# Kernel optimization log

Measured on AMD Instinct MI355X. Metric: run time of the kernel, lower is better.

## Reference

```python
import jax, jax.numpy as jnp
import numpy as np

NUM_HEADS = 16
HEAD_DIM = 64
D_MODEL = NUM_HEADS * HEAD_DIM


def setup_inputs() -> dict:
    key = jax.random.key(0)
    k1, k2, k3 = jax.random.split(key, 3)
    N, T = 2, 2048
    x = jax.random.normal(k1, (N, T, D_MODEL), dtype=jnp.float32)
    mask = jnp.ones((N, T), dtype=jnp.float32)
    # fused QKV projection params (Dense: H*D*3 outputs)
    W_qkv = jax.random.normal(k2, (D_MODEL, D_MODEL * 3), dtype=jnp.float32) * (D_MODEL ** -0.5)
    b_qkv = jnp.zeros((D_MODEL * 3,), dtype=jnp.float32)
    return {"x": x, "mask": mask, "W_qkv": W_qkv, "b_qkv": b_qkv}


def reference(x, mask, W_qkv, b_qkv):
    N, T, _ = x.shape
    H, D = NUM_HEADS, HEAD_DIM
    qkv = x @ W_qkv + b_qkv                       # [N, T, H*D*3]
    qkv = qkv.reshape(N, T, H, D, 3)
    qkv = jnp.transpose(qkv, (4, 0, 2, 1, 3))     # [3, N, H, T, D]
    q, k, v = qkv[0], qkv[1], qkv[2]
    logits = jnp.einsum('bhqd,bhkd->bhqk', q, k) / (D ** 0.5)  # [N, H, T, T]
    # NOTE: original masks along the QUERY axis (broadcast over keys)
    logits = logits + (1.0 - mask)[:, None, :, None] * -1e9
    w = jax.nn.softmax(logits, axis=-1)
    out = jnp.einsum('bhqk,bhkd->bhqd', w, v)     # [N, H, T, D]
    out = jnp.transpose(out, (0, 2, 1, 3)).reshape(N, T, H * D)
    return out
```

## Files before the change

### kernel.cpp

```cpp
#include <hip/hip_runtime.h>
#include <hip/hip_bf16.h>
#include <stdint.h>

#define NHEADS 16
#define HDIM   64
#define DMODEL 1024
#define SEQ    2048
#define NB     2
#define MTOT   (NB*SEQ)
#define NTOT   (3*DMODEL)
#define KTOT   DMODEL

#define QSCALE 0.18033688011112042f

typedef __attribute__((ext_vector_type(8)))  short          bf16x8;
typedef __attribute__((ext_vector_type(4)))  float          f32x4;
typedef __attribute__((ext_vector_type(8)))  unsigned short u16x8;

__device__ __forceinline__ unsigned short f2bf(float f) {
  unsigned u = __builtin_bit_cast(unsigned, f);
  u += 0x7fffu + ((u >> 16) & 1u);
  return (unsigned short)(u >> 16);
}

__device__ __forceinline__ f32x4 vmax4(f32x4 a, f32x4 b) {
  f32x4 r;
  r[0]=fmaxf(a[0],b[0]); r[1]=fmaxf(a[1],b[1]);
  r[2]=fmaxf(a[2],b[2]); r[3]=fmaxf(a[3],b[3]);
  return r;
}

__device__ __forceinline__ void async_copy16(void* lds, const void* g) {
  __builtin_amdgcn_global_load_lds(
      (const __attribute__((address_space(1))) unsigned int*)g,
      (__attribute__((address_space(3))) unsigned int*)lds, 16, 0, 0);
}

__global__ void convert_x_kernel(const float* __restrict__ x,
                                 unsigned short* __restrict__ xb) {
  int i = blockIdx.x * 256 + threadIdx.x;
  const f32x4* xv = reinterpret_cast<const f32x4*>(x);
  f32x4 a = xv[2*i];
  f32x4 b = xv[2*i + 1];
  u16x8 r;
  r[0]=f2bf(a[0]); r[1]=f2bf(a[1]); r[2]=f2bf(a[2]); r[3]=f2bf(a[3]);
  r[4]=f2bf(b[0]); r[5]=f2bf(b[1]); r[6]=f2bf(b[2]); r[7]=f2bf(b[3]);
  reinterpret_cast<u16x8*>(xb)[i] = r;
}

__global__ void transpose_w_kernel(const float* __restrict__ W,
                                   unsigned short* __restrict__ Wt) {
  __shared__ float tile[64][65];
  int j0 = blockIdx.x * 64;
  int k0 = blockIdx.y * 64;
  int tid = threadIdx.x;
  int lr = tid >> 6;
  int lc = tid & 63;
  #pragma unroll
  for (int i = 0; i < 16; ++i) {
    int r = i*4 + lr;
    tile[r][lc] = W[(size_t)(k0 + r)*NTOT + j0 + lc];
  }
  __syncthreads();
  #pragma unroll
  for (int i = 0; i < 16; ++i) {
    int jr = i*4 + lr;
    int j  = j0 + jr;
    int oc = (j % 3)*DMODEL + (j / 3);
    Wt[(size_t)oc*KTOT + k0 + lc] = f2bf(tile[lc][jr]);
  }
}

#define BM 128
#define BN 128
#define BK2 32
#define NBX (NTOT/BN)
#define NBY (MTOT/BM)
#define EPSTRIDE 136
__launch_bounds__(256)
__global__ void qkv_gemm_kernel(const unsigned short* __restrict__ xb,
                                const unsigned short* __restrict__ wt,
                                const float* __restrict__ bqkv,
                                unsigned short* __restrict__ Qb,
                                unsigned short* __restrict__ Kb,
                                unsigned short* __restrict__ Vt) {
  __shared__ __align__(16) unsigned char gsm[128*EPSTRIDE*2];
  unsigned short* As = (unsigned short*)gsm;
  unsigned short* Bs = (unsigned short*)(gsm + 16384);
  unsigned short* Ep = (unsigned short*)gsm;

  int tid = threadIdx.x;
  int w = tid >> 6, l = tid & 63;
  int m0 = blockIdx.y * BM;
  int n0 = blockIdx.x * BN;
  int ln = l & 15, lg = l >> 4;
  int wm = (w >> 1) * 64;
  int wn = (w & 1) * 64;

  f32x4 acc[4][4];
  const f32x4 zero4 = {0.f, 0.f, 0.f, 0.f};
  #pragma unroll
  for (int i = 0; i < 4; ++i)
    #pragma unroll
    for (int j = 0; j < 4; ++j) acc[i][j] = zero4;

  #define STAGE2(BUF, KT)                                                     \
  do {                                                                        \
    _Pragma("unroll")                                                         \
    for (int i = 0; i < 2; ++i) {                                             \
      int row  = i*64 + w*16 + (l >> 2);                                      \
      int seg  = (l & 3) ^ ((row >> 1) & 3);                                  \
      async_copy16(gsm + (BUF)*8192 + i*4096 + w*1024,                        \
                   &xb[(size_t)(m0 + row)*KTOT + (KT)*BK2 + seg*8]);          \
      async_copy16(gsm + 16384 + (BUF)*8192 + i*4096 + w*1024,                \
                   &wt[(size_t)(n0 + row)*KTOT + (KT)*BK2 + seg*8]);          \
    }                                                                         \
  } while (0)

  STAGE2(0, 0);
  asm volatile("s_waitcnt vmcnt(0)" ::: "memory");
  __syncthreads();

  for (int kt = 0; kt < KTOT/BK2; ++kt) {
    int cur = kt & 1;
    if (kt < KTOT/BK2 - 1) STAGE2(cur ^ 1, kt + 1);

    bf16x8 af[4], bfr[4];
    #pragma unroll
    for (int mi = 0; mi < 4; ++mi) {
      int ra = wm + mi*16 + ln;
      af[mi] = *reinterpret_cast<const bf16x8*>(
          &As[cur*4096 + ra*BK2 + ((lg ^ ((ra >> 1) & 3)) << 3)]);
    }
    #pragma unroll
    for (int ni = 0; ni < 4; ++ni) {
      int rb = wn + ni*16 + ln;
      bfr[ni] = *reinterpret_cast<const bf16x8*>(
          &Bs[cur*4096 + rb*BK2 + ((lg ^ ((rb >> 1) & 3)) << 3)]);
    }
    #pragma unroll
    for (int mi = 0; mi < 4; ++mi)
      #pragma unroll
      for (int ni = 0; ni < 4; ++ni)
        acc[mi][ni] = __builtin_amdgcn_mfma_f32_16x16x32_bf16(af[mi], bfr[ni], acc[mi][ni], 0, 0, 0);

    __syncthreads();
  }
  #undef STAGE2

  int r4 = lg * 4;
  if (n0 >= 2*DMODEL) {
    int hd0 = n0 - 2*DMODEL;
    #pragma unroll
    for (int mi = 0; mi < 4; ++mi) {
      #pragma unroll
      for (int ni = 0; ni < 4; ++ni) {
        int col = wn + ni*16 + ln;
        float bias = bqkv[(hd0 + col)*3 + 2];
        int rb = wm + mi*16 + r4;
        ushort4 pk4;
        pk4.x = f2bf(acc[mi][ni][0] + bias);
        pk4.y = f2bf(acc[mi][ni][1] + bias);
        pk4.z = f2bf(acc[mi][ni][2] + bias);
        pk4.w = f2bf(acc[mi][ni][3] + bias);
        *reinterpret_cast<ushort4*>(&Ep[col*EPSTRIDE + rb]) = pk4;
      }
    }
    __syncthreads();
    int n = m0 >> 11, t0 = m0 & 2047;
    #pragma unroll
    for (int pass = 0; pass < 8; ++pass) {
      int hdl = pass*16 + (tid >> 4);
      int seg = tid & 15;
      bf16x8 v = *reinterpret_cast<const bf16x8*>(&Ep[hdl*EPSTRIDE + seg*8]);
      int hd = hd0 + hdl, h = hd >> 6, d = hd & 63;
      *reinterpret_cast<bf16x8*>(
          &Vt[(((size_t)(n*NHEADS + h)*HDIM + d) << 11) + t0 + seg*8]) = v;
    }
  } else {
    #pragma unroll
    for (int mi = 0; mi < 4; ++mi) {
      #pragma unroll
      for (int ni = 0; ni < 4; ++ni) {
        int nc = n0 + wn + ni*16 + ln;
        int c  = nc >> 10;
        int hd = nc & 1023;
        int h = hd >> 6, d = hd & 63;
        float bias = bqkv[hd*3 + c];
        float qs = (c == 0) ? QSCALE : 1.0f;
        #pragma unroll
        for (int j = 0; j < 4; ++j) {
          int m = m0 + wm + mi*16 + r4 + j;
          int n = m >> 11, t = m & 2047;
          unsigned short val = f2bf((acc[mi][ni][j] + bias) * qs);
          size_t nh = (size_t)(n*NHEADS + h);
          if (c == 0) Qb[((nh*SEQ + t) << 6) + d] = val;
          else        Kb[((nh*SEQ + t) << 6) + d] = val;
        }
      }
    }
  }
}

#define PROW    88
#define POFF    49152
#define PBYTES  2816
#define OREGION 4352
__launch_bounds__(512)
__global__ void attn_kernel(const unsigned short* __restrict__ Qb,
                            const unsigned short* __restrict__ Kb,
                            const unsigned short* __restrict__ Vt,
                            float* __restrict__ out) {
  __shared__ __align__(16) unsigned char smem[POFF + 8*PBYTES];
  int tid = threadIdx.x;
  int w = tid >> 6, l = tid & 63;
  int ln = l & 15, lg = l >> 4;

  unsigned short* Pw  = (unsigned short*)(smem + POFF + w * PBYTES);
  float*          obw = (float*)         (smem + w * OREGION);

  int fid  = blockIdx.x;
  int xcd  = fid & 7, idx = fid >> 3;
  int bh   = xcd * 4 + (idx >> 4);
  int qblk = idx & 15;
  int q0   = qblk * 128 + w * 16;

  const unsigned short* Qh = Qb + (size_t)bh * SEQ * HDIM;
  const unsigned short* Kh = Kb + (size_t)bh * SEQ * HDIM;
  const unsigned short* Vh = Vt + (size_t)bh * HDIM * SEQ;

  int srow = w*8 + (l >> 3);
  int sseg = (l & 7) ^ (srow & 7);

  bf16x8 qf[2];
  #pragma unroll
  for (int dw = 0; dw < 2; ++dw)
    qf[dw] = *reinterpret_cast<const bf16x8*>(&Qh[(size_t)(q0 + ln)*HDIM + dw*32 + lg*8]);

  const f32x4 zero4 = {0.f, 0.f, 0.f, 0.f};
  f32x4 o[4];
  #pragma unroll
  for (int db = 0; db < 4; ++db) o[db] = zero4;
  f32x4 psum4 = zero4;
  float mrow = -INFINITY;
  f32x4 sA[4], sB[4];

  int xorE = (ln & 7) << 3;
  int coff0 = (((     lg*8) ^ xorE)) * 2;
  int coff1 = (((32 + lg*8) ^ xorE)) * 2;
  int rbyte = ln * 128;
  const unsigned char* kv0 = smem + rbyte + coff0;
  const unsigned char* kv1 = smem + rbyte + coff1;

  #define STAGE(BUF, KEY0)                                                    \
  do {                                                                        \
    async_copy16(smem + (BUF)*16384 + w*1024,                                 \
                 &Kh[(size_t)((KEY0) + srow)*HDIM + sseg*8]);                 \
    async_copy16(smem + (BUF)*16384 + 8192 + w*1024,                          \
                 &Vh[(size_t)srow*SEQ + (KEY0) + sseg*8]);                    \
  } while (0)

  #define QKT(CUR, SCUR)                                                      \
  do {                                                                        \
    _Pragma("unroll")                                                         \
    for (int kb = 0; kb < 4; ++kb) {                                          \
      bf16x8 k0 = *reinterpret_cast<const bf16x8*>(kv0 + (CUR)*16384 + kb*2048);\
      bf16x8 k1 = *reinterpret_cast<const bf16x8*>(kv1 + (CUR)*16384 + kb*2048);\
      f32x4 t0 = __builtin_amdgcn_mfma_f32_16x16x32_bf16(k0, qf[0], zero4, 0, 0, 0);\
      SCUR[kb] = __builtin_amdgcn_mfma_f32_16x16x32_bf16(k1, qf[1], t0,    0, 0, 0);\
    }                                                                         \
  } while (0)

  #define SMPV(SPREV, PRV)                                                    \
  do {                                                                        \
    f32x4 m4 = vmax4(vmax4(SPREV[0], SPREV[1]), vmax4(SPREV[2], SPREV[3]));   \
    float localmax = fmaxf(fmaxf(fmaxf(m4[0], m4[1]), m4[2]), m4[3]);         \
    if (!__all(localmax <= mrow + 8.f)) {                                     \
      float pm = localmax;                                                    \
      pm = fmaxf(pm, __shfl_xor(pm, 16));                                     \
      pm = fmaxf(pm, __shfl_xor(pm, 32));                                     \
      float mn  = fmaxf(mrow, pm);                                            \
      float scl = __builtin_amdgcn_exp2f(mrow - mn);                          \
      mrow = mn;                                                              \
      psum4 *= scl;                                                           \
      _Pragma("unroll")                                                       \
      for (int db = 0; db < 4; ++db)                                          \
        _Pragma("unroll")                                                     \
        for (int r = 0; r < 4; ++r) o[db][r] *= scl;                          \
    }                                                                         \
    _Pragma("unroll")                                                         \
    for (int kb = 0; kb < 4; ++kb) {                                          \
      _Pragma("unroll")                                                       \
      for (int r = 0; r < 4; ++r)                                             \
        SPREV[kb][r] = __builtin_amdgcn_exp2f(SPREV[kb][r] - mrow);           \
      psum4 += SPREV[kb];                                                     \
    }                                                                         \
    _Pragma("unroll")                                                         \
    for (int kb = 0; kb < 4; ++kb) {                                          \
      uint2 pk;                                                               \
      asm("v_cvt_pk_bf16_f32 %0, %1, %2" : "=v"(pk.x) : "v"(SPREV[kb][0]), "v"(SPREV[kb][1]));\
      asm("v_cvt_pk_bf16_f32 %0, %1, %2" : "=v"(pk.y) : "v"(SPREV[kb][2]), "v"(SPREV[kb][3]));\
      *reinterpret_cast<uint2*>(&Pw[ln*PROW + kb*16 + 4*lg]) = pk;            \
    }                                                                         \
    _Pragma("unroll")                                                         \
    for (int kw = 0; kw < 2; ++kw) {                                          \
      bf16x8 pb = *reinterpret_cast<const bf16x8*>(&Pw[ln*PROW + kw*32 + lg*8]);\
      const unsigned char* vb = (kw == 0) ? kv0 : kv1;                        \
      __builtin_amdgcn_s_setprio(1);                                          \
      _Pragma("unroll")                                                       \
      for (int db = 0; db < 4; ++db) {                                        \
        bf16x8 vfr = *reinterpret_cast<const bf16x8*>(                        \
            vb + (PRV)*16384 + 8192 + db*2048);                               \
        o[db] = __builtin_amdgcn_mfma_f32_16x16x32_bf16(vfr, pb, o[db], 0, 0, 0);\
      }                                                                       \
      __builtin_amdgcn_s_setprio(0);                                          \
    }                                                                         \
  } while (0)

  #define ENDTILE                                                             \
  do {                                                                        \
    asm volatile("s_waitcnt vmcnt(0)" ::: "memory");                          \
    __builtin_amdgcn_s_barrier();                                             \
    asm volatile("" ::: "memory");                                            \
  } while (0)

  #define FULL(KV, CUR, PRV, NXT, SPREV, SCUR)                                \
  do {                                                                        \
    STAGE(NXT, ((KV) + 1) * 64);                                              \
    QKT(CUR, SCUR);                                                           \
    SMPV(SPREV, PRV);                                                         \
    ENDTILE;                                                                  \
  } while (0)

  STAGE(0, 0);
  ENDTILE;
  STAGE(1, 64);
  QKT(0, sA);
  ENDTILE;

  for (int t = 1; t < 31; t += 6) {
    FULL(t + 0, 1, 0, 2, sA, sB);
    FULL(t + 1, 2, 1, 0, sB, sA);
    FULL(t + 2, 0, 2, 1, sA, sB);
    FULL(t + 3, 1, 0, 2, sB, sA);
    FULL(t + 4, 2, 1, 0, sA, sB);
    FULL(t + 5, 0, 2, 1, sB, sA);
  }

  QKT(1, sB);
  SMPV(sA, 0);
  ENDTILE;
  SMPV(sB, 1);

  __syncthreads();

  #undef FULL
  #undef ENDTILE
  #undef SMPV
  #undef QKT
  #undef STAGE

  float ls = (psum4[0] + psum4[1]) + (psum4[2] + psum4[3]);
  ls += __shfl_xor(ls, 16);
  ls += __shfl_xor(ls, 32);
  float inv = 1.f / ls;

  #pragma unroll
  for (int db = 0; db < 4; ++db)
    #pragma unroll
    for (int r = 0; r < 4; ++r)
      obw[ln*68 + db*16 + 4*lg + r] = o[db][r] * inv;
  asm volatile("s_waitcnt lgkmcnt(0)" ::: "memory");
  int n = bh >> 4, h = bh & 15;
  #pragma unroll
  for (int p = 0; p < 4; ++p) {
    int q = p*4 + lg;
    f32x4 vv = *reinterpret_cast<const f32x4*>(&obw[q*68 + ln*4]);
    *reinterpret_cast<f32x4*>(
        &out[((size_t)(n*SEQ + q0 + q))*DMODEL + h*HDIM + ln*4]) = vv;
  }
}

extern "C" void kernel_launch(void* const* d_in, const int* in_sizes, int n_in,
                              void* d_out, int out_size, void* d_ws, size_t ws_size,
                              hipStream_t stream) {
  const float* x    = (const float*)d_in[0];
  const float* Wq   = (const float*)d_in[2];
  const float* bq   = (const float*)d_in[3];
  float* out = (float*)d_out;

  unsigned short* xb = (unsigned short*)d_ws;
  unsigned short* wt = xb + (size_t)MTOT*KTOT;
  unsigned short* Qb = wt + (size_t)NTOT*KTOT;
  unsigned short* Kb = Qb + (size_t)NB*NHEADS*SEQ*HDIM;
  unsigned short* Vt = Kb + (size_t)NB*NHEADS*SEQ*HDIM;

  convert_x_kernel<<<(MTOT*KTOT/8)/256, 256, 0, stream>>>(x, xb);
  transpose_w_kernel<<<dim3(NTOT/64, KTOT/64), 256, 0, stream>>>(Wq, wt);
  qkv_gemm_kernel<<<dim3(NBX, NBY), 256, 0, stream>>>(xb, wt, bq, Qb, Kb, Vt);
  attn_kernel<<<512, 512, 0, stream>>>(Qb, Kb, Vt, out);
}
```

Before: 107.8 us.

## Load V fragments directly from global into registers instead of staging via LDS

V tiles are no longer staged through shared memory with async copies. Each lane now loads its V MFMA operands straight from global memory into registers at the start of every iteration, so only K stays in the triple-buffered LDS ring and the LDS footprint is halved. This cuts LDS traffic and shared-memory size, which could allow higher occupancy. The cost is per-wave redundant global loads of V (all 8 waves in a block read the same V tile) and exposed global latency, since the loads are issued in the same iteration that consumes them.

Measured after the change: 209.5 us. +94.4%, slower.

```diff
diff --git a/kernel.cpp b/kernel.cpp
--- a/kernel.cpp
+++ b/kernel.cpp
@@ -203,7 +203,7 @@
 }
 
 #define PROW    88
-#define POFF    49152
+#define POFF    24576
 #define PBYTES  2816
 #define OREGION 4352
 __launch_bounds__(512)
@@ -237,6 +237,11 @@
   for (int dw = 0; dw < 2; ++dw)
     qf[dw] = *reinterpret_cast<const bf16x8*>(&Qh[(size_t)(q0 + ln)*HDIM + dw*32 + lg*8]);
 
+  const unsigned short* vrow0 = Vh + (size_t)(0*16 + ln)*SEQ + lg*8;
+  const unsigned short* vrow1 = Vh + (size_t)(1*16 + ln)*SEQ + lg*8;
+  const unsigned short* vrow2 = Vh + (size_t)(2*16 + ln)*SEQ + lg*8;
+  const unsigned short* vrow3 = Vh + (size_t)(3*16 + ln)*SEQ + lg*8;
+
   const f32x4 zero4 = {0.f, 0.f, 0.f, 0.f};
   f32x4 o[4];
   #pragma unroll
@@ -244,6 +249,7 @@
   f32x4 psum4 = zero4;
   float mrow = -INFINITY;
   f32x4 sA[4], sB[4];
+  bf16x8 vf[2][4];
 
   int xorE = (ln & 7) << 3;
   int coff0 = (((     lg*8) ^ xorE)) * 2;
@@ -254,24 +260,33 @@
 
   #define STAGE(BUF, KEY0)                                                    \
   do {                                                                        \
-    async_copy16(smem + (BUF)*16384 + w*1024,                                 \
+    async_copy16(smem + (BUF)*8192 + w*1024,                                  \
                  &Kh[(size_t)((KEY0) + srow)*HDIM + sseg*8]);                 \
-    async_copy16(smem + (BUF)*16384 + 8192 + w*1024,                          \
-                 &Vh[(size_t)srow*SEQ + (KEY0) + sseg*8]);                    \
+  } while (0)
+
+  #define LOADV(KEY0)                                                         \
+  do {                                                                        \
+    _Pragma("unroll")                                                         \
+    for (int kw = 0; kw < 2; ++kw) {                                          \
+      vf[kw][0] = *reinterpret_cast<const bf16x8*>(vrow0 + (KEY0) + kw*32);   \
+      vf[kw][1] = *reinterpret_cast<const bf16x8*>(vrow1 + (KEY0) + kw*32);   \
+      vf[kw][2] = *reinterpret_cast<const bf16x8*>(vrow2 + (KEY0) + kw*32);   \
+      vf[kw][3] = *reinterpret_cast<const bf16x8*>(vrow3 + (KEY0) + kw*32);   \
+    }                                                                         \
   } while (0)
 
   #define QKT(CUR, SCUR)                                                      \
   do {                                                                        \
     _Pragma("unroll")                                                         \
     for (int kb = 0; kb < 4; ++kb) {                                          \
-      bf16x8 k0 = *reinterpret_cast<const bf16x8*>(kv0 + (CUR)*16384 + kb*2048);\
-      bf16x8 k1 = *reinterpret_cast<const bf16x8*>(kv1 + (CUR)*16384 + kb*2048);\
+      bf16x8 k0 = *reinterpret_cast<const bf16x8*>(kv0 + (CUR)*8192 + kb*2048);\
+      bf16x8 k1 = *reinterpret_cast<const bf16x8*>(kv1 + (CUR)*8192 + kb*2048);\
       f32x4 t0 = __builtin_amdgcn_mfma_f32_16x16x32_bf16(k0, qf[0], zero4, 0, 0, 0);\
       SCUR[kb] = __builtin_amdgcn_mfma_f32_16x16x32_bf16(k1, qf[1], t0,    0, 0, 0);\
     }                                                                         \
   } while (0)
 
-  #define SMPV(SPREV, PRV)                                                    \
+  #define SMPV(SPREV)                                                         \
   do {                                                                        \
     f32x4 m4 = vmax4(vmax4(SPREV[0], SPREV[1]), vmax4(SPREV[2], SPREV[3]));   \
     float localmax = fmaxf(fmaxf(fmaxf(m4[0], m4[1]), m4[2]), m4[3]);         \
@@ -305,14 +320,10 @@
     _Pragma("unroll")                                                         \
     for (int kw = 0; kw < 2; ++kw) {                                          \
       bf16x8 pb = *reinterpret_cast<const bf16x8*>(&Pw[ln*PROW + kw*32 + lg*8]);\
-      const unsigned char* vb = (kw == 0) ? kv0 : kv1;                        \
       __builtin_amdgcn_s_setprio(1);                                          \
       _Pragma("unroll")                                                       \
-      for (int db = 0; db < 4; ++db) {                                        \
-        bf16x8 vfr = *reinterpret_cast<const bf16x8*>(                        \
-            vb + (PRV)*16384 + 8192 + db*2048);                               \
-        o[db] = __builtin_amdgcn_mfma_f32_16x16x32_bf16(vfr, pb, o[db], 0, 0, 0);\
-      }                                                                       \
+      for (int db = 0; db < 4; ++db)                                          \
+        o[db] = __builtin_amdgcn_mfma_f32_16x16x32_bf16(vf[kw][db], pb, o[db], 0, 0, 0);\
       __builtin_amdgcn_s_setprio(0);                                          \
     }                                                                         \
   } while (0)
@@ -324,11 +335,12 @@
     asm volatile("" ::: "memory");                                            \
   } while (0)
 
-  #define FULL(KV, CUR, PRV, NXT, SPREV, SCUR)                                \
+  #define FULL(KV, CUR, NXT, SPREV, SCUR)                                     \
   do {                                                                        \
     STAGE(NXT, ((KV) + 1) * 64);                                              \
+    LOADV(((KV) - 1) * 64);                                                   \
     QKT(CUR, SCUR);                                                           \
-    SMPV(SPREV, PRV);                                                         \
+    SMPV(SPREV);                                                              \
     ENDTILE;                                                                  \
   } while (0)
 
@@ -339,18 +351,20 @@
   ENDTILE;
 
   for (int t = 1; t < 31; t += 6) {
-    FULL(t + 0, 1, 0, 2, sA, sB);
-    FULL(t + 1, 2, 1, 0, sB, sA);
-    FULL(t + 2, 0, 2, 1, sA, sB);
-    FULL(t + 3, 1, 0, 2, sB, sA);
-    FULL(t + 4, 2, 1, 0, sA, sB);
-    FULL(t + 5, 0, 2, 1, sB, sA);
-  }
-
+    FULL(t + 0, 1, 2, sA, sB);
+    FULL(t + 1, 2, 0, sB, sA);
+    FULL(t + 2, 0, 1, sA, sB);
+    FULL(t + 3, 1, 2, sB, sA);
+    FULL(t + 4, 2, 0, sA, sB);
+    FULL(t + 5, 0, 1, sB, sA);
+  }
+
+  LOADV(30 * 64);
   QKT(1, sB);
-  SMPV(sA, 0);
+  SMPV(sA);
   ENDTILE;
-  SMPV(sB, 1);
+  LOADV(31 * 64);
+  SMPV(sB);
 
   __syncthreads();
 
@@ -358,6 +372,7 @@
   #undef ENDTILE
   #undef SMPV
   #undef QKT
+  #undef LOADV
   #undef STAGE
 
   float ls = (psum4[0] + psum4[1]) + (psum4[2] + psum4[3]);
```
